# Kernel optimization log

Hardware: AMD Instinct MI355X
Metric: run time of the kernel (lower is better)

## Reference

```python
import jax, jax.numpy as jnp
import numpy as np

EPS = 1e-8
NEG = -float(2 ** 31)

B, N, D = 8, 2048, 256  # batch, nodes, input_dim == output_dim


def setup_inputs() -> dict:
    key = jax.random.key(0)
    ks = jax.random.split(key, 8)
    x = jax.random.normal(ks[0], (B, N, D), dtype=jnp.float32)
    x_topic = jax.random.normal(ks[1], (B, N, D), dtype=jnp.float32)
    adj_mask = jax.random.randint(ks[2], (B, N, N), 0, 2, dtype=jnp.int32)
    s = 1.0 / np.sqrt(D)
    W = jax.random.uniform(ks[3], (D, D), minval=-s, maxval=s, dtype=jnp.float32)
    # GRUCell params (torch layout: [3*H, in] with gate order r, z, n)
    W_ih = jax.random.uniform(ks[4], (3 * D, D), minval=-s, maxval=s, dtype=jnp.float32)
    W_hh = jax.random.uniform(ks[5], (3 * D, D), minval=-s, maxval=s, dtype=jnp.float32)
    b_ih = jax.random.uniform(ks[6], (3 * D,), minval=-s, maxval=s, dtype=jnp.float32)
    b_hh = jax.random.uniform(ks[7], (3 * D,), minval=-s, maxval=s, dtype=jnp.float32)
    return {"adj_mask": adj_mask, "x": x, "x_topic": x_topic,
            "W": W, "W_ih": W_ih, "W_hh": W_hh, "b_ih": b_ih, "b_hh": b_hh}


def _gru_cell(inp, h, W_ih, W_hh, b_ih, b_hh):
    # torch.nn.GRUCell math, gate order (r, z, n)
    gi = inp @ W_ih.T + b_ih
    gh = h @ W_hh.T + b_hh
    i_r, i_z, i_n = jnp.split(gi, 3, axis=-1)
    h_r, h_z, h_n = jnp.split(gh, 3, axis=-1)
    r = jax.nn.sigmoid(i_r + h_r)
    z = jax.nn.sigmoid(i_z + h_z)
    n = jnp.tanh(i_n + r * h_n)
    return (1.0 - z) * n + z * h


def reference(adj_mask, x, x_topic, W, W_ih, W_hh, b_ih, b_hh):
    # Wh: [B, N, H]
    Wh = jnp.einsum('bnd,dh->bnh', x, W)
    # pairwise cosine similarity via normalized gram matrix (no N x N x D intermediate)
    nrm = jnp.linalg.norm(x_topic, axis=-1)            # [B, N]
    dots = jnp.einsum('bnd,bmd->bnm', x_topic, x_topic)
    e = dots / jnp.maximum(nrm[:, :, None] * nrm[:, None, :], EPS)
    scores = jnp.where(adj_mask > 0, e, NEG)
    attention = jax.nn.softmax(scores, axis=-1)        # [B, N, N]
    graph_out = jnp.einsum('bnm,bmh->bnh', attention, Wh)
    out = _gru_cell(graph_out, x, W_ih, W_hh, b_ih, b_hh)
    return out
```

## Files before the change

kernel.cpp:

```cpp
#include <hip/hip_runtime.h>
#include <hip/hip_bf16.h>

#define B_ 8
#define N_ 2048
#define D_ 256

using bf16 = __hip_bfloat16;
typedef short v8s __attribute__((ext_vector_type(8)));
typedef float v4f __attribute__((ext_vector_type(4)));
typedef float v16f __attribute__((ext_vector_type(16)));
typedef unsigned int u32;
typedef unsigned long long u64;

__device__ __forceinline__ v4f mfma16(v8s a, v8s b, v4f c) {
  return __builtin_amdgcn_mfma_f32_16x16x32_bf16(a, b, c, 0, 0, 0);
}
__device__ __forceinline__ v16f mfma32(v8s a, v8s b, v16f c) {
  return __builtin_amdgcn_mfma_f32_32x32x16_bf16(a, b, c, 0, 0, 0);
}
__device__ __forceinline__ v8s ldb8(const bf16* p) {
  return *reinterpret_cast<const v8s*>(p);
}
__device__ __forceinline__ void glds16(const void* g, void* l) {
  __builtin_amdgcn_global_load_lds((const __attribute__((address_space(1))) u32*)g,
                                   (__attribute__((address_space(3))) u32*)l, 16, 0, 0);
}
__device__ __forceinline__ unsigned short f2bu(float f) {
  bf16 b = __float2bfloat16(f);
  return *reinterpret_cast<unsigned short*>(&b);
}
__device__ __forceinline__ float bs2f(short s) {
  union { u32 i; float f; } v; v.i = ((u32)(unsigned short)s) << 16; return v.f;
}
__device__ __forceinline__ float lo16(u32 u) { union {u32 i; float f;} v; v.i = u << 16; return v.f; }
__device__ __forceinline__ float hi16(u32 u) { union {u32 i; float f;} v; v.i = u & 0xffff0000u; return v.f; }
__device__ __forceinline__ u32 pack2(float a, float b) {
  return (u32)f2bu(a) | ((u32)f2bu(b) << 16);
}
__device__ __forceinline__ float fsigmoid(float x) { return 1.0f / (1.0f + __expf(-x)); }
__device__ __forceinline__ float ftanh(float x) {
  float ax = fabsf(x);
  float t = __expf(-2.0f * ax);
  float r = (1.0f - t) / (1.0f + t);
  return copysignf(r, x);
}

__global__ __launch_bounds__(256) void k_cvt(const float* __restrict__ src,
                                             bf16* __restrict__ dst, int n4) {
  int i = blockIdx.x * 256 + threadIdx.x;
  if (i >= n4) return;
  float4 v = reinterpret_cast<const float4*>(src)[i];
  ushort4 o;
  o.x = f2bu(v.x); o.y = f2bu(v.y); o.z = f2bu(v.z); o.w = f2bu(v.w);
  reinterpret_cast<ushort4*>(dst)[i] = o;
}

__global__ __launch_bounds__(256) void k_cvtn(const float* __restrict__ xt,
                                              bf16* __restrict__ dst,
                                              float* __restrict__ rnorm) {
  int i = blockIdx.x * 256 + threadIdx.x;
  int lane = threadIdx.x & 63;
  float4 v = reinterpret_cast<const float4*>(xt)[i];
  ushort4 o;
  o.x = f2bu(v.x); o.y = f2bu(v.y); o.z = f2bu(v.z); o.w = f2bu(v.w);
  reinterpret_cast<ushort4*>(dst)[i] = o;
  float s = v.x * v.x + v.y * v.y + v.z * v.z + v.w * v.w;
#pragma unroll
  for (int off = 32; off > 0; off >>= 1) s += __shfl_xor(s, off);
  if (lane == 0) rnorm[i >> 6] = 1.0f / fmaxf(sqrtf(s), 1e-8f);
}

__global__ __launch_bounds__(256) void k_prep(const float* __restrict__ W,
                                              bf16* __restrict__ Wt,
                                              const float* __restrict__ Wih,
                                              bf16* __restrict__ Wih16,
                                              const float* __restrict__ Whh,
                                              bf16* __restrict__ Whh16) {
  int blk = blockIdx.x;
  if (blk < 256) {
    int idx = blk * 256 + threadIdx.x;
    int d = idx >> 8, h = idx & 255;
    Wt[h * 256 + d] = __float2bfloat16(W[idx]);
  } else if (blk < 448) {
    int i = (blk - 256) * 256 + threadIdx.x;
    float4 v = reinterpret_cast<const float4*>(Wih)[i];
    ushort4 o;
    o.x = f2bu(v.x); o.y = f2bu(v.y); o.z = f2bu(v.z); o.w = f2bu(v.w);
    reinterpret_cast<ushort4*>(Wih16)[i] = o;
  } else {
    int i = (blk - 448) * 256 + threadIdx.x;
    float4 v = reinterpret_cast<const float4*>(Whh)[i];
    ushort4 o;
    o.x = f2bu(v.x); o.y = f2bu(v.y); o.z = f2bu(v.z); o.w = f2bu(v.w);
    reinterpret_cast<ushort4*>(Whh16)[i] = o;
  }
}

__global__ __launch_bounds__(256) void k_pack(const int* __restrict__ adj,
                                              u64* __restrict__ adjp) {
  int wid = (blockIdx.x * 256 + threadIdx.x) >> 6;
  int lane = threadIdx.x & 63;
  const int G = B_ * N_ * (N_ / 64);
#pragma unroll 4
  for (int g = wid; g < G; g += 16384) {
    int v = adj[(size_t)g * 64 + lane];
    u64 m = __ballot(v > 0);
    if (lane == 0) adjp[g] = m;
  }
}

__global__ __launch_bounds__(256) void k_wht(const bf16* __restrict__ x,
                                             const bf16* __restrict__ Wt,
                                             bf16* __restrict__ WhT) {
  int wid = blockIdx.x * 4 + (threadIdx.x >> 6);
  int lane = threadIdx.x & 63, lr = lane & 15, quad = lane >> 4;
  int b = wid >> 9;
  int rem = wid & 511;
  int h0 = (rem >> 5) << 4;
  int m0 = (rem & 31) << 6;

  v8s a[8];
  const bf16* arow = Wt + (size_t)(h0 + lr) * D_ + quad * 8;
#pragma unroll
  for (int ks = 0; ks < 8; ks++) a[ks] = ldb8(arow + ks * 32);

  const bf16* xb = x + (size_t)b * N_ * D_;
#pragma unroll
  for (int mt = 0; mt < 4; mt++) {
    v4f acc = {0.f, 0.f, 0.f, 0.f};
    const bf16* brow = xb + (size_t)(m0 + mt * 16 + lr) * D_ + quad * 8;
#pragma unroll
    for (int ks = 0; ks < 8; ks++) acc = mfma16(a[ks], ldb8(brow + ks * 32), acc);
    bf16* o = WhT + ((size_t)b * D_ + h0 + quad * 4) * N_ + m0 + mt * 16 + lr;
#pragma unroll
    for (int r = 0; r < 4; r++) o[(size_t)r * N_] = __float2bfloat16(acc[r]);
  }
}

__global__ __launch_bounds__(256, 2) void k_attn(const bf16* __restrict__ xt,
                                                 const u32* __restrict__ adj32,
                                                 const bf16* __restrict__ WhT,
                                                 const float* __restrict__ rnorm,
                                                 bf16* __restrict__ po,
                                                 float* __restrict__ pls) {
  __shared__ __align__(16) bf16 xts[2][32 * 256];
  __shared__ __align__(16) bf16 whs[2][256 * 32];
  __shared__ __align__(16) bf16 pbuf[4][32 * 40];
  __shared__ float rns[512];

  const int tid = threadIdx.x;
  const int w = tid >> 6, lane = tid & 63;
  const int l5 = lane >> 5, l31 = lane & 31;
  const int b = blockIdx.x & 7;
  const int nt = (blockIdx.x >> 3) & 15;
  const int mh = blockIdx.x >> 7;
  const int n0w = nt * 128 + w * 32;
  const int mbase = mh * 512;

  const bf16* xtb = xt + (size_t)b * N_ * D_;
  const bf16* whb = WhT + (size_t)b * D_ * N_;

  if (tid < 128)
    ((float4*)rns)[tid] = ((const float4*)(rnorm + b * N_ + mbase))[tid];

  v8s q[16];
  {
    const bf16* qrow = xtb + (size_t)(n0w + l31) * D_ + l5 * 8;
#pragma unroll
    for (int kt = 0; kt < 16; kt++) q[kt] = ldb8(qrow + kt * 16);
  }
  const float rq = rnorm[b * N_ + n0w + l31];
  const u32* arow = adj32 + (size_t)(b * N_ + n0w + l31) * 64 + mh * 16;

  auto stage = [&](int d, int m0) {
    const char* gx = (const char*)(xtb + (size_t)m0 * D_);
    char* lx = ((char*)xts[d]) + w * 4096;
#pragma unroll
    for (int j = 0; j < 4; j++) {
      int m = w * 8 + j * 2 + l5;
      int gg = l31 ^ (m & 7);
      glds16(gx + (size_t)m * 512 + gg * 16, lx + j * 1024);
    }
    char* lw = ((char*)whs[d]) + w * 4096;
#pragma unroll
    for (int j = 0; j < 4; j++) {
      int h = w * 64 + j * 16 + (lane >> 2);
      int g = (lane & 3) ^ ((lane >> 2) & 3);
      glds16((const char*)(whb + (size_t)h * N_ + m0) + g * 16, lw + j * 1024);
    }
  };

  v16f o[8];
#pragma unroll
  for (int t = 0; t < 8; t++) o[t] = (v16f)(0.f);
  float lsum = 0.f;

  u32 mword = arow[0];
  stage(0, mbase);

#pragma unroll 1
  for (int ii = 0; ii < 16; ii++) {
    const int d = ii & 1;
    __syncthreads();
    if (ii + 1 < 16) stage(1 - d, mbase + (ii + 1) * 32);

    v16f s = (v16f)(0.f);
    const bf16* xb = xts[d] + l31 * 256;
#pragma unroll
    for (int kt = 0; kt < 16; kt++) {
      int g = ((kt * 2 + l5) ^ (lane & 7)) * 8;
      s = mfma32(q[kt], ldb8(xb + g), s);
    }

    u32 mnext = (ii + 1 < 16) ? arow[ii + 1] : 0u;
    float rm = rns[ii * 32 + l31];

    bf16* pb = pbuf[w];
#pragma unroll
    for (int j = 0; j < 16; j++) {
      int row = (j & 3) + 8 * (j >> 2) + 4 * l5;
      u32 mw = __shfl(mword, row);
      float rnj = __shfl(rq, row);
      float p = ((mw >> l31) & 1u) ? __expf(s[j] * rnj * rm) : 0.f;
      pb[row * 40 + l31] = __float2bfloat16(p);
    }
    mword = mnext;

    v8s pa0 = ldb8(pb + l31 * 40 + l5 * 8);
    v8s pa1 = ldb8(pb + l31 * 40 + 16 + l5 * 8);
#pragma unroll
    for (int e = 0; e < 8; e++) lsum += bs2f(pa0[e]) + bs2f(pa1[e]);

#pragma unroll
    for (int ht = 0; ht < 8; ht++) {
      const bf16* wb = whs[d] + (ht * 32 + l31) * 32;
      int g0 = (l5 ^ (l31 & 3)) * 8;
      int g1 = ((2 + l5) ^ (l31 & 3)) * 8;
      o[ht] = mfma32(pa0, ldb8(wb + g0), o[ht]);
      o[ht] = mfma32(pa1, ldb8(wb + g1), o[ht]);
    }
  }

  lsum += __shfl_xor(lsum, 32);
  if (lane < 32) pls[(size_t)mh * (B_ * N_) + b * N_ + n0w + l31] = lsum;

  bf16* pob = po + (size_t)mh * ((size_t)B_ * N_ * D_) + ((size_t)b * N_ + n0w) * D_;
#pragma unroll
  for (int ht = 0; ht < 8; ht++) {
#pragma unroll
    for (int j = 0; j < 16; j++) {
      int row = (j & 3) + 8 * (j >> 2) + 4 * l5;
      pob[(size_t)row * D_ + ht * 32 + l31] = __float2bfloat16(o[ht][j]);
    }
  }
}

__global__ __launch_bounds__(256) void k_comb(const bf16* __restrict__ po,
                                              const float* __restrict__ pls,
                                              bf16* __restrict__ gout) {
  int idx = blockIdx.x * 256 + threadIdx.x;
  int row = idx >> 5;
  const int R = B_ * N_;
  float inv = 1.0f / (pls[row] + pls[R + row] + pls[2 * R + row] + pls[3 * R + row]);
  const size_t S = (size_t)B_ * N_ * D_ / 8;
  const uint4* p = (const uint4*)po;
  uint4 a = p[idx], c = p[idx + S], e = p[idx + 2 * S], f = p[idx + 3 * S];
  uint4 o;
  o.x = pack2((lo16(a.x)+lo16(c.x)+lo16(e.x)+lo16(f.x)) * inv,
              (hi16(a.x)+hi16(c.x)+hi16(e.x)+hi16(f.x)) * inv);
  o.y = pack2((lo16(a.y)+lo16(c.y)+lo16(e.y)+lo16(f.y)) * inv,
              (hi16(a.y)+hi16(c.y)+hi16(e.y)+hi16(f.y)) * inv);
  o.z = pack2((lo16(a.z)+lo16(c.z)+lo16(e.z)+lo16(f.z)) * inv,
              (hi16(a.z)+hi16(c.z)+hi16(e.z)+hi16(f.z)) * inv);
  o.w = pack2((lo16(a.w)+lo16(c.w)+lo16(e.w)+lo16(f.w)) * inv,
              (hi16(a.w)+hi16(c.w)+hi16(e.w)+hi16(f.w)) * inv);
  reinterpret_cast<uint4*>(gout)[idx] = o;
}

__global__ __launch_bounds__(256) void k_gru(const bf16* __restrict__ gout,
                                             const bf16* __restrict__ x16,
                                             const bf16* __restrict__ Wih,
                                             const bf16* __restrict__ Whh,
                                             const float* __restrict__ bih,
                                             const float* __restrict__ bhh,
                                             const float* __restrict__ x32,
                                             float* __restrict__ out) {
  int wid = blockIdx.x * 4 + (threadIdx.x >> 6);
  int lane = threadIdx.x & 63, lr = lane & 15, quad = lane >> 4;
  int rs = wid >> 4;
  int col0 = (wid & 15) << 4;
  int row0 = rs << 6;
  int col = col0 + lr;

  float bi[3], bh[3];
#pragma unroll
  for (int g = 0; g < 3; g++) {
    bi[g] = bih[g * 256 + col];
    bh[g] = bhh[g * 256 + col];
  }
  v4f aI[3][4], aH[3][4];
#pragma unroll
  for (int g = 0; g < 3; g++)
#pragma unroll
    for (int rt = 0; rt < 4; rt++) {
      aI[g][rt] = (v4f){0, 0, 0, 0};
      aH[g][rt] = (v4f){0, 0, 0, 0};
    }

#pragma unroll 2
  for (int ks = 0; ks < 8; ks++) {
    int k0 = ks * 32 + quad * 8;
    v8s wI[3], wH[3];
#pragma unroll
    for (int g = 0; g < 3; g++) {
      wI[g] = ldb8(Wih + (size_t)(g * 256 + col0 + lr) * 256 + k0);
      wH[g] = ldb8(Whh + (size_t)(g * 256 + col0 + lr) * 256 + k0);
    }
#pragma unroll
    for (int rt = 0; rt < 4; rt++) {
      v8s aG = ldb8(gout + (size_t)(row0 + rt * 16 + lr) * 256 + k0);
      v8s aX = ldb8(x16 + (size_t)(row0 + rt * 16 + lr) * 256 + k0);
#pragma unroll
      for (int g = 0; g < 3; g++) {
        aI[g][rt] = mfma16(aG, wI[g], aI[g][rt]);
        aH[g][rt] = mfma16(aX, wH[g], aH[g][rt]);
      }
    }
  }

#pragma unroll
  for (int rt = 0; rt < 4; rt++) {
    int rowb = row0 + rt * 16 + quad * 4;
#pragma unroll
    for (int r = 0; r < 4; r++) {
      float ir  = aI[0][rt][r] + bi[0];
      float iz  = aI[1][rt][r] + bi[1];
      float in_ = aI[2][rt][r] + bi[2];
      float hr  = aH[0][rt][r] + bh[0];
      float hz  = aH[1][rt][r] + bh[1];
      float hn  = aH[2][rt][r] + bh[2];
      float rg = fsigmoid(ir + hr);
      float zg = fsigmoid(iz + hz);
      float ng = ftanh(in_ + rg * hn);
      float hv = x32[(size_t)(rowb + r) * 256 + col];
      out[(size_t)(rowb + r) * 256 + col] = (1.0f - zg) * ng + zg * hv;
    }
  }
}

extern "C" void kernel_launch(void* const* d_in, const int* in_sizes, int n_in,
                              void* d_out, int out_size, void* d_ws, size_t ws_size,
                              hipStream_t stream) {
  const int*   adj = (const int*)d_in[0];
  const float* x   = (const float*)d_in[1];
  const float* xt  = (const float*)d_in[2];
  const float* W   = (const float*)d_in[3];
  const float* Wih = (const float*)d_in[4];
  const float* Whh = (const float*)d_in[5];
  const float* bih = (const float*)d_in[6];
  const float* bhh = (const float*)d_in[7];
  float* out = (float*)d_out;

  char* ws = (char*)d_ws;
  bf16*  xb16   = (bf16*)(ws);
  bf16*  xtb16  = (bf16*)(ws + (8u << 20));
  bf16*  gob    = (bf16*)(ws + (16u << 20));
  bf16*  WhT    = (bf16*)(ws + (24u << 20));
  bf16*  Wt     = (bf16*)(ws + (32u << 20));
  bf16*  Wih16  = (bf16*)(ws + (32u << 20) + (128u << 10));
  bf16*  Whh16  = (bf16*)(ws + (32u << 20) + (512u << 10));
  float* rnorm  = (float*)(ws + (32u << 20) + (896u << 10));
  u64*   adjp   = (u64*)  (ws + (32u << 20) + (960u << 10));
  bf16*  po     = (bf16*) (ws + (40u << 20));
  float* pls    = (float*)(ws + (72u << 20));

  const int nBND4 = B_ * N_ * D_ / 4;
  k_pack<<<4096, 256, 0, stream>>>(adj, adjp);
  k_cvt<<<nBND4 / 256, 256, 0, stream>>>(x, xb16, nBND4);
  k_cvtn<<<nBND4 / 256, 256, 0, stream>>>(xt, xtb16, rnorm);
  k_prep<<<640, 256, 0, stream>>>(W, Wt, Wih, Wih16, Whh, Whh16);
  k_wht<<<1024, 256, 0, stream>>>(xb16, Wt, WhT);
  k_attn<<<512, 256, 0, stream>>>(xtb16, (const u32*)adjp, WhT, rnorm, po, pls);
  k_comb<<<2048, 256, 0, stream>>>(po, pls, gob);
  k_gru<<<1024, 256, 0, stream>>>(gob, xb16, Wih16, Whh16, bih, bhh, x, out);
}
```

Before: 423.0 us.

## Pre-normalize x_topic rows and transpose adjacency bitmask to drop per-element shuffles

The x_topic rows are now normalized before the bf16 conversion, so the attention kernel's dot products are already cosine similarities. This removes the rnorm buffer, its shared-memory staging, and the two scalings inside the exp. The adjacency is repacked into a transposed bitmask (32 query rows per word, indexed by key column), so each lane reads its own mask word instead of shuffling one per element. LDS swizzle patterns are also adjusted to reduce bank conflicts. Rounding normalized values to bf16 slightly changes numerics, and the new pack kernel reads the int adjacency with a different access pattern.

```diff
diff --git a/kernel.cpp b/kernel.cpp
--- a/kernel.cpp
+++ b/kernel.cpp
@@ -10,7 +10,6 @@
 typedef float v4f __attribute__((ext_vector_type(4)));
 typedef float v16f __attribute__((ext_vector_type(16)));
 typedef unsigned int u32;
-typedef unsigned long long u64;
 
 __device__ __forceinline__ v4f mfma16(v8s a, v8s b, v4f c) {
   return __builtin_amdgcn_mfma_f32_16x16x32_bf16(a, b, c, 0, 0, 0);
@@ -56,18 +55,17 @@
 }
 
 __global__ __launch_bounds__(256) void k_cvtn(const float* __restrict__ xt,
-                                              bf16* __restrict__ dst,
-                                              float* __restrict__ rnorm) {
+                                              bf16* __restrict__ dst) {
   int i = blockIdx.x * 256 + threadIdx.x;
-  int lane = threadIdx.x & 63;
   float4 v = reinterpret_cast<const float4*>(xt)[i];
+  float s = v.x * v.x + v.y * v.y + v.z * v.z + v.w * v.w;
+#pragma unroll
+  for (int off = 32; off > 0; off >>= 1) s += __shfl_xor(s, off);
+  float rinv = 1.0f / fmaxf(sqrtf(s), 1e-8f);
   ushort4 o;
-  o.x = f2bu(v.x); o.y = f2bu(v.y); o.z = f2bu(v.z); o.w = f2bu(v.w);
+  o.x = f2bu(v.x * rinv); o.y = f2bu(v.y * rinv);
+  o.z = f2bu(v.z * rinv); o.w = f2bu(v.w * rinv);
   reinterpret_cast<ushort4*>(dst)[i] = o;
-  float s = v.x * v.x + v.y * v.y + v.z * v.z + v.w * v.w;
-#pragma unroll
-  for (int off = 32; off > 0; off >>= 1) s += __shfl_xor(s, off);
-  if (lane == 0) rnorm[i >> 6] = 1.0f / fmaxf(sqrtf(s), 1e-8f);
 }
 
 __global__ __launch_bounds__(256) void k_prep(const float* __restrict__ W,
@@ -96,17 +94,23 @@
   }
 }
 
-__global__ __launch_bounds__(256) void k_pack(const int* __restrict__ adj,
-                                              u64* __restrict__ adjp) {
-  int wid = (blockIdx.x * 256 + threadIdx.x) >> 6;
-  int lane = threadIdx.x & 63;
-  const int G = B_ * N_ * (N_ / 64);
+__global__ __launch_bounds__(256) void k_packT(const int* __restrict__ adj,
+                                               u32* __restrict__ maskT) {
+  int bi = blockIdx.x;
+  int bg = bi >> 1, half = bi & 1;
+  const int* base = adj + (size_t)bg * 32 * 2048;
+  int c0 = half * 1024 + threadIdx.x * 4;
+  u32 w0 = 0, w1 = 0, w2 = 0, w3 = 0;
 #pragma unroll 4
-  for (int g = wid; g < G; g += 16384) {
-    int v = adj[(size_t)g * 64 + lane];
-    u64 m = __ballot(v > 0);
-    if (lane == 0) adjp[g] = m;
-  }
+  for (int r = 0; r < 32; r++) {
+    int4 v = *reinterpret_cast<const int4*>(base + r * 2048 + c0);
+    w0 |= (u32)(v.x > 0) << r;
+    w1 |= (u32)(v.y > 0) << r;
+    w2 |= (u32)(v.z > 0) << r;
+    w3 |= (u32)(v.w > 0) << r;
+  }
+  uint4 o; o.x = w0; o.y = w1; o.z = w2; o.w = w3;
+  *reinterpret_cast<uint4*>(maskT + (size_t)bg * 2048 + c0) = o;
 }
 
 __global__ __launch_bounds__(256) void k_wht(const bf16* __restrict__ x,
@@ -137,16 +141,14 @@
   }
 }
 
-__global__ __launch_bounds__(256, 2) void k_attn(const bf16* __restrict__ xt,
-                                                 const u32* __restrict__ adj32,
+__global__ __launch_bounds__(256, 2) void k_attn(const bf16* __restrict__ xtn,
+                                                 const u32* __restrict__ maskT,
                                                  const bf16* __restrict__ WhT,
-                                                 const float* __restrict__ rnorm,
                                                  bf16* __restrict__ po,
                                                  float* __restrict__ pls) {
   __shared__ __align__(16) bf16 xts[2][32 * 256];
   __shared__ __align__(16) bf16 whs[2][256 * 32];
   __shared__ __align__(16) bf16 pbuf[4][32 * 40];
-  __shared__ float rns[512];
 
   const int tid = threadIdx.x;
   const int w = tid >> 6, lane = tid & 63;
@@ -157,11 +159,8 @@
   const int n0w = nt * 128 + w * 32;
   const int mbase = mh * 512;
 
-  const bf16* xtb = xt + (size_t)b * N_ * D_;
+  const bf16* xtb = xtn + (size_t)b * N_ * D_;
   const bf16* whb = WhT + (size_t)b * D_ * N_;
-
-  if (tid < 128)
-    ((float4*)rns)[tid] = ((const float4*)(rnorm + b * N_ + mbase))[tid];
 
   v8s q[16];
   {
@@ -169,8 +168,7 @@
 #pragma unroll
     for (int kt = 0; kt < 16; kt++) q[kt] = ldb8(qrow + kt * 16);
   }
-  const float rq = rnorm[b * N_ + n0w + l31];
-  const u32* arow = adj32 + (size_t)(b * N_ + n0w + l31) * 64 + mh * 16;
+  const u32* mrow = maskT + ((size_t)(b * 64 + nt * 4 + w)) * 2048 + mbase + l31;
 
   auto stage = [&](int d, int m0) {
     const char* gx = (const char*)(xtb + (size_t)m0 * D_);
@@ -185,7 +183,7 @@
 #pragma unroll
     for (int j = 0; j < 4; j++) {
       int h = w * 64 + j * 16 + (lane >> 2);
-      int g = (lane & 3) ^ ((lane >> 2) & 3);
+      int g = (lane & 3) ^ ((lane >> 3) & 3);
       glds16((const char*)(whb + (size_t)h * N_ + m0) + g * 16, lw + j * 1024);
     }
   };
@@ -195,7 +193,7 @@
   for (int t = 0; t < 8; t++) o[t] = (v16f)(0.f);
   float lsum = 0.f;
 
-  u32 mword = arow[0];
+  u32 mword = mrow[0];
   stage(0, mbase);
 
 #pragma unroll 1
@@ -203,25 +201,21 @@
     const int d = ii & 1;
     __syncthreads();
     if (ii + 1 < 16) stage(1 - d, mbase + (ii + 1) * 32);
+    u32 mnext = (ii + 1 < 16) ? mrow[(ii + 1) * 32] : 0u;
 
     v16f s = (v16f)(0.f);
     const bf16* xb = xts[d] + l31 * 256;
 #pragma unroll
     for (int kt = 0; kt < 16; kt++) {
-      int g = ((kt * 2 + l5) ^ (lane & 7)) * 8;
+      int g = ((kt * 2 + l5) ^ (l31 & 7)) * 8;
       s = mfma32(q[kt], ldb8(xb + g), s);
     }
-
-    u32 mnext = (ii + 1 < 16) ? arow[ii + 1] : 0u;
-    float rm = rns[ii * 32 + l31];
 
     bf16* pb = pbuf[w];
 #pragma unroll
     for (int j = 0; j < 16; j++) {
       int row = (j & 3) + 8 * (j >> 2) + 4 * l5;
-      u32 mw = __shfl(mword, row);
-      float rnj = __shfl(rq, row);
-      float p = ((mw >> l31) & 1u) ? __expf(s[j] * rnj * rm) : 0.f;
+      float p = ((mword >> row) & 1u) ? __expf(s[j]) : 0.f;
       pb[row * 40 + l31] = __float2bfloat16(p);
     }
     mword = mnext;
@@ -234,10 +228,10 @@
 #pragma unroll
     for (int ht = 0; ht < 8; ht++) {
       const bf16* wb = whs[d] + (ht * 32 + l31) * 32;
-      int g0 = (l5 ^ (l31 & 3)) * 8;
-      int g1 = ((2 + l5) ^ (l31 & 3)) * 8;
-      o[ht] = mfma32(pa0, ldb8(wb + g0), o[ht]);
-      o[ht] = mfma32(pa1, ldb8(wb + g1), o[ht]);
+      int s0 = (l5 ^ ((l31 >> 1) & 3)) * 8;
+      int s1 = ((2 + l5) ^ ((l31 >> 1) & 3)) * 8;
+      o[ht] = mfma32(pa0, ldb8(wb + s0), o[ht]);
+      o[ht] = mfma32(pa1, ldb8(wb + s1), o[ht]);
     }
   }
 
@@ -363,24 +357,23 @@
 
   char* ws = (char*)d_ws;
   bf16*  xb16   = (bf16*)(ws);
-  bf16*  xtb16  = (bf16*)(ws + (8u << 20));
+  bf16*  xtn    = (bf16*)(ws + (8u << 20));
   bf16*  gob    = (bf16*)(ws + (16u << 20));
   bf16*  WhT    = (bf16*)(ws + (24u << 20));
   bf16*  Wt     = (bf16*)(ws + (32u << 20));
   bf16*  Wih16  = (bf16*)(ws + (32u << 20) + (128u << 10));
   bf16*  Whh16  = (bf16*)(ws + (32u << 20) + (512u << 10));
-  float* rnorm  = (float*)(ws + (32u << 20) + (896u << 10));
-  u64*   adjp   = (u64*)  (ws + (32u << 20) + (960u << 10));
+  u32*   maskT  = (u32*)  (ws + (32u << 20) + (960u << 10));
   bf16*  po     = (bf16*) (ws + (40u << 20));
   float* pls    = (float*)(ws + (72u << 20));
 
   const int nBND4 = B_ * N_ * D_ / 4;
-  k_pack<<<4096, 256, 0, stream>>>(adj, adjp);
+  k_packT<<<1024, 256, 0, stream>>>(adj, maskT);
   k_cvt<<<nBND4 / 256, 256, 0, stream>>>(x, xb16, nBND4);
-  k_cvtn<<<nBND4 / 256, 256, 0, stream>>>(xt, xtb16, rnorm);
+  k_cvtn<<<nBND4 / 256, 256, 0, stream>>>(xt, xtn);
   k_prep<<<640, 256, 0, stream>>>(W, Wt, Wih, Wih16, Whh, Whh16);
   k_wht<<<1024, 256, 0, stream>>>(xb16, Wt, WhT);
-  k_attn<<<512, 256, 0, stream>>>(xtb16, (const u32*)adjp, WhT, rnorm, po, pls);
+  k_attn<<<512, 256, 0, stream>>>(xtn, maskT, WhT, po, pls);
   k_comb<<<2048, 256, 0, stream>>>(po, pls, gob);
   k_gru<<<1024, 256, 0, stream>>>(gob, xb16, Wih16, Whh16, bih, bhh, x, out);
 }
```

Result: faster. 396.3 us (-6.3%).
